# Kernel optimization log

Hardware: AMD Instinct MI355X
Metric: run time of the kernel (lower is better)

## Reference

```python
import math
import jax, jax.numpy as jnp
import numpy as np

N_HEAD = 16
HEAD_DIM = 128


def _rope(x, cos, sin):
    # x: (B,T,H,D); cos,sin: (T,1,D/2) broadcast over B,H
    d = x.shape[-1] // 2
    x1, x2 = x[..., :d], x[..., d:]
    return jnp.concatenate([x1 * cos + x2 * sin, -x1 * sin + x2 * cos], axis=-1)


def _rms_norm(x, eps=1e-6):
    return x * jax.lax.rsqrt(jnp.mean(x * x, axis=-1, keepdims=True) + eps)


def setup_inputs() -> dict:
    key = jax.random.key(0)
    ks = jax.random.split(key, 9)
    B, T, C = 2, 2048, 2048
    scale = 1.0 / math.sqrt(C)
    return {
        "x": jax.random.normal(ks[0], (B, T, C), jnp.float32),
        "ve": jax.random.normal(ks[1], (B, T, C), jnp.float32),
        "Wq": jax.random.normal(ks[2], (C, C), jnp.float32) * scale,
        "Wk": jax.random.normal(ks[3], (C, C), jnp.float32) * scale,
        "Wv": jax.random.normal(ks[4], (C, C), jnp.float32) * scale,
        "Wproj": jax.random.normal(ks[5], (C, C), jnp.float32) * scale,
        "Wgate": jax.random.normal(ks[6], (N_HEAD, 12), jnp.float32) * (1.0 / math.sqrt(12.0)),
        "cos": jax.random.uniform(ks[7], (T, 1, HEAD_DIM // 2), jnp.float32),
        "sin": jax.random.uniform(ks[8], (T, 1, HEAD_DIM // 2), jnp.float32),
        "window_left": 1024,
    }


def reference(x, ve, Wq, Wk, Wv, Wproj, Wgate, cos, sin, window_left):
    B, T, C = x.shape
    H, D = N_HEAD, HEAD_DIM

    # Linear projections (torch Linear: x @ W.T)
    q = (x @ Wq.T).reshape(B, T, H, D)
    k = (x @ Wk.T).reshape(B, T, H, D)
    v = (x @ Wv.T).reshape(B, T, H, D)

    # value-embedding gating (has_ve layer)
    gate = 3.0 * jax.nn.sigmoid(x[..., :12] @ Wgate.T)  # (B,T,H)
    v = v + gate[..., None] * ve.reshape(B, T, H, D)

    # rope + qk rms-norm * 1.2
    q = _rms_norm(_rope(q, cos, sin)) * 1.2
    k = _rms_norm(_rope(k, cos, sin)) * 1.2

    # windowed causal mask
    row = jnp.arange(T)[:, None]
    col = jnp.arange(T)[None, :]
    mask = row >= col
    if 0 < window_left < T:
        mask = mask & (row - col <= window_left)
    bias = jnp.where(mask, 0.0, -1e9).astype(x.dtype)  # (T,T)

    scale = 1.0 / math.sqrt(D)
    att = jnp.einsum("bqhd,bkhd->bhqk", q, k) * scale + bias[None, None]
    att = jax.nn.softmax(att, axis=-1)
    y = jnp.einsum("bhqk,bkhd->bqhd", att, v).reshape(B, T, H * D)
    return y @ Wproj.T
```

## Files before the change

### kernel.cpp

```cpp
#include <hip/hip_runtime.h>
#include <hip/hip_bf16.h>
#include <cstdint>

#define N_HEAD 16
#define HEAD_DIM 128

typedef __bf16 bf16;
typedef __bf16 bf16x8 __attribute__((ext_vector_type(8)));
typedef __bf16 bf16x4 __attribute__((ext_vector_type(4)));
typedef float f32x4 __attribute__((ext_vector_type(4)));

__device__ __forceinline__ void gload_lds16(const void* g, void* l) {
  auto gp = reinterpret_cast<const __attribute__((address_space(1))) char*>(
      reinterpret_cast<uintptr_t>(g));
  auto lp = reinterpret_cast<__attribute__((address_space(3))) char*>(
      reinterpret_cast<uintptr_t>(l));
  __builtin_amdgcn_global_load_lds(gp, lp, 16, 0, 0);
}

__global__ __launch_bounds__(256) void cvt_all(
    const float* __restrict__ x, const float* __restrict__ Wq,
    const float* __restrict__ Wk, const float* __restrict__ Wv,
    const float* __restrict__ Wp, bf16* __restrict__ xb,
    bf16* __restrict__ wqkv, bf16* __restrict__ wpb, int nx4, int nw4) {
  const int z = blockIdx.z;
  const float* in;
  bf16* out;
  int n4;
  if (z == 0)      { in = x;  out = xb;  n4 = nx4; }
  else if (z == 1) { in = Wq; out = wqkv;                     n4 = nw4; }
  else if (z == 2) { in = Wk; out = wqkv + (size_t)nw4 * 4;   n4 = nw4; }
  else if (z == 3) { in = Wv; out = wqkv + (size_t)nw4 * 8;   n4 = nw4; }
  else             { in = Wp; out = wpb;  n4 = nw4; }
  const int i = blockIdx.x * 256 + threadIdx.x;
  if (i >= n4) return;
  const float4 f = reinterpret_cast<const float4*>(in)[i];
  bf16x4 o;
  o.x = (bf16)f.x; o.y = (bf16)f.y; o.z = (bf16)f.z; o.w = (bf16)f.w;
  reinterpret_cast<bf16x4*>(out)[i] = o;
}

__global__ __launch_bounds__(512, 2) void gemm256(
    const bf16* __restrict__ A, const bf16* __restrict__ Bt,
    bf16* __restrict__ C, int M, int N, int K) {
  __shared__ __align__(16) char sA[2][32768];
  __shared__ __align__(16) char sB[2][32768];

  const int nwgy = M >> 8;
  const int nwg = gridDim.x;
  const int q8 = nwg >> 3;
  const int wgid = (blockIdx.x & 7) * q8 + (blockIdx.x >> 3);
  const int by = wgid % nwgy;
  const int bx = wgid / nwgy;

  const int tid = threadIdx.x;
  const int lane = tid & 63;
  const int wave = tid >> 6;
  const int wm = (wave >> 2) << 7;
  const int wn = (wave & 3) << 6;
  const int lr = lane & 15;
  const int lk16 = (lane >> 4) << 4;
  const int sx = (lr & 7) << 4;

  const bf16* Ab = A + (size_t)by * 256 * K;
  const bf16* Bb = Bt + (size_t)bx * 256 * K;

  int srow[2], scol[2];
#pragma unroll
  for (int pp = 0; pp < 2; ++pp) {
    const int o = pp * 8192 + tid * 16;
    srow[pp] = o >> 7;
    scol[pp] = (o & 127) ^ ((srow[pp] & 7) << 4);
  }

  auto stageA = [&](int buf, int half, int k0) {
#pragma unroll
    for (int pp = 0; pp < 2; ++pp)
      gload_lds16(Ab + (size_t)(half * 128 + srow[pp]) * K + k0 + (scol[pp] >> 1),
                  sA[buf] + half * 16384 + pp * 8192 + tid * 16);
  };
  auto stageB = [&](int buf, int half, int k0) {
#pragma unroll
    for (int pp = 0; pp < 2; ++pp)
      gload_lds16(Bb + (size_t)(half * 128 + srow[pp]) * K + k0 + (scol[pp] >> 1),
                  sB[buf] + half * 16384 + pp * 8192 + tid * 16);
  };

  f32x4 acc[8][4] = {};
  bf16x8 bF[4][2];

#define VMCNT4                                             \
  asm volatile("s_waitcnt vmcnt(4)" ::: "memory");         \
  __builtin_amdgcn_sched_barrier(0)
#define VMCNT0                                             \
  asm volatile("s_waitcnt vmcnt(0)" ::: "memory");         \
  __builtin_amdgcn_sched_barrier(0)

#define PHASE(BUF, P, STAGE, WAIT)                                             \
  {                                                                            \
    bf16x8 aF[2][2];                                                           \
    if (P == 0) {                                                              \
      _Pragma("unroll") for (int n = 0; n < 4; ++n)                            \
      _Pragma("unroll") for (int ks = 0; ks < 2; ++ks)                         \
        bF[n][ks] = *reinterpret_cast<const bf16x8*>(                          \
            sB[BUF] + (wn + n * 16 + lr) * 128 + ((ks * 64 + lk16) ^ sx));     \
    }                                                                          \
    _Pragma("unroll") for (int mi = 0; mi < 2; ++mi)                           \
    _Pragma("unroll") for (int ks = 0; ks < 2; ++ks)                           \
      aF[mi][ks] = *reinterpret_cast<const bf16x8*>(                           \
          sA[BUF] + (wm + (P * 2 + mi) * 16 + lr) * 128 +                      \
          ((ks * 64 + lk16) ^ sx));                                            \
    STAGE;                                                                     \
    WAIT;                                                                      \
    __builtin_amdgcn_s_barrier();                                              \
    __builtin_amdgcn_s_setprio(1);                                             \
    _Pragma("unroll") for (int ks = 0; ks < 2; ++ks)                           \
    _Pragma("unroll") for (int mi = 0; mi < 2; ++mi)                           \
    _Pragma("unroll") for (int n = 0; n < 4; ++n)                              \
      acc[P * 2 + mi][n] = __builtin_amdgcn_mfma_f32_16x16x32_bf16(            \
          aF[mi][ks], bF[n][ks], acc[P * 2 + mi][n], 0, 0, 0);                 \
    __builtin_amdgcn_s_setprio(0);                                             \
    __builtin_amdgcn_s_barrier();                                              \
  }

  const int nIt = K >> 7;

  stageB(0, 0, 0); stageB(0, 1, 0);
  stageA(0, 0, 0); stageA(0, 1, 0);
  stageB(1, 0, 64); stageB(1, 1, 64);
  VMCNT4;
  __builtin_amdgcn_s_barrier();

  int k0 = 0;
  for (int it = 0; it < nIt - 1; ++it, k0 += 128) {
    PHASE(0, 0, stageA(1, 0, k0 + 64), );
    PHASE(0, 1, stageA(1, 1, k0 + 64), );
    PHASE(0, 2, stageB(0, 0, k0 + 128), );
    PHASE(0, 3, stageB(0, 1, k0 + 128), VMCNT4);
    PHASE(1, 0, stageA(0, 0, k0 + 128), );
    PHASE(1, 1, stageA(0, 1, k0 + 128), );
    PHASE(1, 2, stageB(1, 0, k0 + 192), );
    PHASE(1, 3, stageB(1, 1, k0 + 192), VMCNT4);
  }
  PHASE(0, 0, stageA(1, 0, k0 + 64), );
  PHASE(0, 1, stageA(1, 1, k0 + 64), );
  PHASE(0, 2, , );
  PHASE(0, 3, , VMCNT0);
  PHASE(1, 0, , );
  PHASE(1, 1, , );
  PHASE(1, 2, , );
  PHASE(1, 3, , );
#undef PHASE
#undef VMCNT4
#undef VMCNT0

  const int orow = by * 256 + wm + (lane >> 4) * 4;
  const int ocol = bx * 256 + wn + lr;
#pragma unroll
  for (int m = 0; m < 8; ++m)
#pragma unroll
    for (int n = 0; n < 4; ++n)
#pragma unroll
      for (int r = 0; r < 4; ++r)
        C[(size_t)(orow + m * 16 + r) * N + (ocol + n * 16)] = (bf16)acc[m][n][r];
}

template <typename OutT>
__global__ __launch_bounds__(512, 2) void gemm128(
    const bf16* __restrict__ A, const bf16* __restrict__ Bt,
    OutT* __restrict__ C, int M, int Ncols, int K, int nOff) {
  __shared__ __align__(16) char sA[2][16384];
  __shared__ __align__(16) char sB[2][32768];

  const int nwgy = M >> 7;
  const int nwg = gridDim.x;
  const int q8 = nwg >> 3;
  const int wgid = (blockIdx.x & 7) * q8 + (blockIdx.x >> 3);
  const int by = wgid % nwgy;
  const int bx = wgid / nwgy;

  const int tid = threadIdx.x;
  const int lane = tid & 63;
  const int wave = tid >> 6;
  const int wn = wave << 5;
  const int lr = lane & 15;
  const int lk16 = (lane >> 4) << 4;
  const int sx = (lr & 7) << 4;

  const bf16* Ab = A + (size_t)by * 128 * K;
  const bf16* Bb = Bt + (size_t)(nOff + bx * 256) * K;

  int srow[2], scol[2];
#pragma unroll
  for (int pp = 0; pp < 2; ++pp) {
    const int o = pp * 8192 + tid * 16;
    srow[pp] = o >> 7;
    scol[pp] = (o & 127) ^ ((srow[pp] & 7) << 4);
  }

  auto stageB = [&](int buf, int half, int k0) {
#pragma unroll
    for (int pp = 0; pp < 2; ++pp)
      gload_lds16(Bb + (size_t)(half * 128 + srow[pp]) * K + k0 + (scol[pp] >> 1),
                  sB[buf] + half * 16384 + pp * 8192 + tid * 16);
  };
  auto stageA = [&](int buf, int half, int k0) {
    const int o = tid * 16;
    const int row = o >> 7;
    const int col = (o & 127) ^ ((row & 7) << 4);
    gload_lds16(Ab + (size_t)(half * 64 + row) * K + k0 + (col >> 1),
                sA[buf] + half * 8192 + o);
  };

  f32x4 acc[8][2] = {};
  bf16x8 bF[2][2];

#define WAITV(n)                                               \
  asm volatile("s_waitcnt vmcnt(" #n ")" ::: "memory");        \
  __builtin_amdgcn_sched_barrier(0)

#define PH128(BUF, P, STAGE, WAIT)                                             \
  {                                                                            \
    bf16x8 aF[2][2];                                                           \
    if (P == 0) {                                                              \
      _Pragma("unroll") for (int n = 0; n < 2; ++n)                            \
      _Pragma("unroll") for (int ks = 0; ks < 2; ++ks)                         \
        bF[n][ks] = *reinterpret_cast<const bf16x8*>(                          \
            sB[BUF] + (wn + n * 16 + lr) * 128 + ((ks * 64 + lk16) ^ sx));     \
    }                                                                          \
    _Pragma("unroll") for (int mi = 0; mi < 2; ++mi)                           \
    _Pragma("unroll") for (int ks = 0; ks < 2; ++ks)                           \
      aF[mi][ks] = *reinterpret_cast<const bf16x8*>(                           \
          sA[BUF] + ((P * 2 + mi) * 16 + lr) * 128 + ((ks * 64 + lk16) ^ sx)); \
    STAGE;                                                                     \
    WAIT;                                                                      \
    __builtin_amdgcn_s_barrier();                                              \
    __builtin_amdgcn_s_setprio(1);                                             \
    _Pragma("unroll") for (int ks = 0; ks < 2; ++ks)                           \
    _Pragma("unroll") for (int mi = 0; mi < 2; ++mi)                           \
    _Pragma("unroll") for (int n = 0; n < 2; ++n)                              \
      acc[P * 2 + mi][n] = __builtin_amdgcn_mfma_f32_16x16x32_bf16(            \
          aF[mi][ks], bF[n][ks], acc[P * 2 + mi][n], 0, 0, 0);                 \
    __builtin_amdgcn_s_setprio(0);                                             \
    __builtin_amdgcn_s_barrier();                                              \
  }

  const int nIt = K >> 7;

  stageB(0, 0, 0); stageB(0, 1, 0);
  stageA(0, 0, 0); stageA(0, 1, 0);
  stageB(1, 0, 64); stageB(1, 1, 64);
  stageA(1, 0, 64);
  WAITV(5);
  __builtin_amdgcn_s_barrier();

  int k0 = 0;
  for (int it = 0; it < nIt - 1; ++it, k0 += 128) {
    PH128(0, 0, stageA(1, 1, k0 + 64), );
    PH128(0, 1, stageB(0, 0, k0 + 128), WAITV(8));
    PH128(0, 2, (stageB(0, 1, k0 + 128), stageA(0, 0, k0 + 128)), );
    PH128(0, 3, , WAITV(6));
    PH128(1, 0, stageA(0, 1, k0 + 128), );
    PH128(1, 1, stageB(1, 0, k0 + 192), WAITV(8));
    PH128(1, 2, (stageB(1, 1, k0 + 192), stageA(1, 0, k0 + 192)), );
    PH128(1, 3, , WAITV(6));
  }
  PH128(0, 0, stageA(1, 1, k0 + 64), );
  PH128(0, 1, , WAITV(6));
  PH128(0, 2, , );
  PH128(0, 3, , WAITV(1));
  PH128(1, 0, , );
  PH128(1, 1, , WAITV(0));
  PH128(1, 2, , );
  PH128(1, 3, , );
#undef PH128
#undef WAITV

  const int orow = by * 128 + (lane >> 4) * 4;
  const int ocol = nOff + bx * 256 + wn + lr;
#pragma unroll
  for (int m = 0; m < 8; ++m)
#pragma unroll
    for (int n = 0; n < 2; ++n)
#pragma unroll
      for (int r = 0; r < 4; ++r)
        C[(size_t)(orow + m * 16 + r) * Ncols + (ocol + n * 16)] = (OutT)acc[m][n][r];
}

__global__ __launch_bounds__(256) void rope_rms(
    bf16* __restrict__ qkv, const float* __restrict__ cs,
    const float* __restrict__ sn, int T) {
  const int C = N_HEAD * HEAD_DIM;
  const int S = 3 * C;
  const int bt = blockIdx.x;
  const int t = bt % T;
  const int wave = threadIdx.x >> 6;
  const int lane = threadIdx.x & 63;
  const int h = blockIdx.y * 4 + wave;
  bf16* p = qkv + (size_t)bt * S + (blockIdx.z ? C : 0) + h * HEAD_DIM;
  const float oscale = blockIdx.z ? 1.2f : 0.15302091809294977f;
  const float c = cs[t * 64 + lane];
  const float s = sn[t * 64 + lane];
  const float x1 = (float)p[lane];
  const float x2 = (float)p[lane + 64];
  const float r1 = x1 * c + x2 * s;
  const float r2 = x2 * c - x1 * s;
  float ss = r1 * r1 + r2 * r2;
#pragma unroll
  for (int m = 1; m < 64; m <<= 1) ss += __shfl_xor(ss, m);
  const float sc = oscale * rsqrtf(ss * (1.0f / 128.0f) + 1e-6f);
  p[lane] = (bf16)(r1 * sc);
  p[lane + 64] = (bf16)(r2 * sc);
}

__global__ __launch_bounds__(256) void gate_transpose(
    const bf16* __restrict__ qkv, const float* __restrict__ x,
    const float* __restrict__ ve, const float* __restrict__ Wg,
    bf16* __restrict__ vT, int T) {
  const int C = N_HEAD * HEAD_DIM;
  const int S = 3 * C;
  const int t0 = blockIdx.x * 64;
  const int c0 = blockIdx.y * 64;
  const int b = blockIdx.z;
  const int h = c0 >> 7;

  __shared__ float gs[64];
  __shared__ __align__(16) bf16 tile[64][72];

  if (threadIdx.x < 64) {
    const float* xr = x + (size_t)(b * T + t0 + threadIdx.x) * C;
    float a = 0.f;
#pragma unroll
    for (int j = 0; j < 12; ++j) a += xr[j] * Wg[h * 12 + j];
    gs[threadIdx.x] = 3.f / (1.f + __expf(-a));
  }
  __syncthreads();

  {
    const int r = threadIdx.x >> 2;
    const int cc = (threadIdx.x & 3) * 16;
    const size_t vrow = (size_t)(b * T + t0 + r) * S + 2 * C + c0 + cc;
    const size_t erow = (size_t)(b * T + t0 + r) * C + c0 + cc;
    bf16x8 a0 = *reinterpret_cast<const bf16x8*>(qkv + vrow);
    bf16x8 a1 = *reinterpret_cast<const bf16x8*>(qkv + vrow + 8);
    const float g = gs[r];
    bf16x8 o0, o1;
#pragma unroll
    for (int i = 0; i < 8; ++i) o0[i] = (bf16)((float)a0[i] + g * ve[erow + i]);
#pragma unroll
    for (int i = 0; i < 8; ++i) o1[i] = (bf16)((float)a1[i] + g * ve[erow + 8 + i]);
    *reinterpret_cast<bf16x8*>(&tile[r][cc]) = o0;
    *reinterpret_cast<bf16x8*>(&tile[r][cc + 8]) = o1;
  }
  __syncthreads();
  {
    const int dr = threadIdx.x >> 2;
    const int tc = (threadIdx.x & 3) * 16;
    bf16x8 o0, o1;
#pragma unroll
    for (int i = 0; i < 8; ++i) o0[i] = tile[tc + i][dr];
#pragma unroll
    for (int i = 0; i < 8; ++i) o1[i] = tile[tc + 8 + i][dr];
    const size_t orow =
        ((size_t)((b * N_HEAD + h) * HEAD_DIM) + (c0 & 127) + dr) * T + t0 + tc;
    *reinterpret_cast<bf16x8*>(vT + orow) = o0;
    *reinterpret_cast<bf16x8*>(vT + orow + 8) = o1;
  }
}

__global__ __launch_bounds__(256, 2) void attn(
    const bf16* __restrict__ qkv, const bf16* __restrict__ vT,
    bf16* __restrict__ y, const int* __restrict__ wptr, int T, int B) {
  const int C = N_HEAD * HEAD_DIM;
  const int S = 3 * C;
  const int nq = T >> 7;
  const int ppx = (B * N_HEAD) >> 3;
  const int bid = blockIdx.x;
  const int xcd = bid & 7;
  const int sl = bid >> 3;
  const int pair = xcd * ppx + sl / nq;
  const int qi = sl % nq;
  const int b = pair / N_HEAD;
  const int h = pair % N_HEAD;
  const int qb = qi * 128;

  const int tid = threadIdx.x;
  const int wave = tid >> 6;
  const int lane = tid & 63;
  const int lm = lane & 15;
  const int quad = lane >> 4;

  const int w = wptr[0];
  const int W = (w > 0 && w < T) ? w : (1 << 30);

  __shared__ __align__(16) bf16 Ks[4][64][32];
  __shared__ __align__(16) bf16 Vs[2][128][32];
  __shared__ __align__(16) bf16 Pb[4][16][72];

  const bf16* kb = qkv + (size_t)b * T * S + C + (size_t)h * HEAD_DIM;
  const bf16* vb = vT + (size_t)((b * N_HEAD + h) * HEAD_DIM) * T;

  const int qt[2] = {qb + wave * 16, qb + 64 + wave * 16};
  bf16x8 qf[2][4];
#pragma unroll
  for (int t = 0; t < 2; ++t) {
    const bf16* qrow = qkv + (size_t)(b * T + qt[t] + lm) * S + h * HEAD_DIM;
#pragma unroll
    for (int c = 0; c < 4; ++c)
      qf[t][c] = *reinterpret_cast<const bf16x8*>(qrow + c * 32 + quad * 8);
  }

  float mrun[2] = {-1e30f, -1e30f}, lrun[2] = {0.f, 0.f};
  f32x4 oacc[2][8] = {};

  int kstart = qb - W;
  if (kstart < 0) kstart = 0;
  kstart &= ~63;
  const int kend = qb + 64;

  const int sr = tid >> 2;
  const int sc = (tid & 3) * 8;

  bf16x8 kpre[4], vpre[4];
  {
    const bf16* kr = kb + (size_t)(kstart + sr) * S + sc;
#pragma unroll
    for (int c = 0; c < 4; ++c)
      kpre[c] = *reinterpret_cast<const bf16x8*>(kr + c * 32);
#pragma unroll
    for (int c2 = 0; c2 < 2; ++c2)
#pragma unroll
      for (int i = 0; i < 2; ++i)
        vpre[c2 * 2 + i] = *reinterpret_cast<const bf16x8*>(
            vb + (size_t)(i * 64 + sr) * T + kstart + c2 * 32 + sc);
  }

  for (int kc = kstart; kc <= kend; kc += 64) {
    __syncthreads();
#pragma unroll
    for (int c = 0; c < 4; ++c)
      *reinterpret_cast<bf16x8*>(&Ks[c][sr][sc]) = kpre[c];
#pragma unroll
    for (int c2 = 0; c2 < 2; ++c2)
#pragma unroll
      for (int i = 0; i < 2; ++i)
        *reinterpret_cast<bf16x8*>(&Vs[c2][i * 64 + sr][sc]) = vpre[c2 * 2 + i];
    __syncthreads();

    if (kc + 64 <= kend) {
      const int kc2 = kc + 64;
      const bf16* kr = kb + (size_t)(kc2 + sr) * S + sc;
#pragma unroll
      for (int c = 0; c < 4; ++c)
        kpre[c] = *reinterpret_cast<const bf16x8*>(kr + c * 32);
#pragma unroll
      for (int c2 = 0; c2 < 2; ++c2)
#pragma unroll
        for (int i = 0; i < 2; ++i)
          vpre[c2 * 2 + i] = *reinterpret_cast<const bf16x8*>(
              vb + (size_t)(i * 64 + sr) * T + kc2 + c2 * 32 + sc);
    }

#pragma unroll
    for (int t = 0; t < 2; ++t) {
      const int q0 = qt[t];
      if (kc > q0 + 15 || kc + 63 < q0 - W) continue;
      const int qr = q0 + lm;

      f32x4 st[4] = {};
#pragma unroll
      for (int g = 0; g < 4; ++g)
#pragma unroll
        for (int c = 0; c < 4; ++c) {
          const bf16x8 kf =
              *reinterpret_cast<const bf16x8*>(&Ks[c][g * 16 + lm][quad * 8]);
          st[g] = __builtin_amdgcn_mfma_f32_16x16x32_bf16(kf, qf[t][c], st[g], 0, 0, 0);
        }
      float mx = -1e30f;
#pragma unroll
      for (int g = 0; g < 4; ++g)
#pragma unroll
        for (int r = 0; r < 4; ++r) {
          const int key = kc + g * 16 + quad * 4 + r;
          const bool valid = (key <= qr) && (qr - key <= W);
          st[g][r] = valid ? st[g][r] : -1e30f;
          mx = fmaxf(mx, st[g][r]);
        }
      mx = fmaxf(mx, __shfl_xor(mx, 16));
      mx = fmaxf(mx, __shfl_xor(mx, 32));
      const float mnew = fmaxf(mrun[t], mx);
      const float alpha = __builtin_amdgcn_exp2f(mrun[t] - mnew);
      mrun[t] = mnew;
      float rs = 0.f;
#pragma unroll
      for (int g = 0; g < 4; ++g) {
        bf16x4 pk;
#pragma unroll
        for (int r = 0; r < 4; ++r) {
          const float p = __builtin_amdgcn_exp2f(st[g][r] - mnew);
          rs += p;
          pk[r] = (bf16)p;
        }
        *reinterpret_cast<bf16x4*>(&Pb[wave][lm][g * 16 + quad * 4]) = pk;
      }
      rs += __shfl_xor(rs, 16);
      rs += __shfl_xor(rs, 32);
      lrun[t] = lrun[t] * alpha + rs;
#pragma unroll
      for (int dc = 0; dc < 8; ++dc)
#pragma unroll
        for (int r = 0; r < 4; ++r) oacc[t][dc][r] *= alpha;
#pragma unroll
      for (int c2 = 0; c2 < 2; ++c2) {
        const bf16x8 pf =
            *reinterpret_cast<const bf16x8*>(&Pb[wave][lm][c2 * 32 + quad * 8]);
#pragma unroll
        for (int dc = 0; dc < 8; ++dc) {
          const bf16x8 vf =
              *reinterpret_cast<const bf16x8*>(&Vs[c2][dc * 16 + lm][quad * 8]);
          oacc[t][dc] = __builtin_amdgcn_mfma_f32_16x16x32_bf16(vf, pf, oacc[t][dc], 0, 0, 0);
        }
      }
    }
  }

#pragma unroll
  for (int t = 0; t < 2; ++t) {
    const float inv = 1.f / lrun[t];
    bf16* yr = y + (size_t)(b * T + qt[t] + lm) * C + h * HEAD_DIM;
#pragma unroll
    for (int dc = 0; dc < 8; ++dc) {
      bf16x4 o;
#pragma unroll
      for (int r = 0; r < 4; ++r) o[r] = (bf16)(oacc[t][dc][r] * inv);
      *reinterpret_cast<bf16x4*>(yr + dc * 16 + quad * 4) = o;
    }
  }
}

extern "C" void kernel_launch(void* const* d_in, const int* in_sizes, int n_in,
                              void* d_out, int out_size, void* d_ws, size_t ws_size,
                              hipStream_t stream) {
  const float* x  = (const float*)d_in[0];
  const float* ve = (const float*)d_in[1];
  const float* Wq = (const float*)d_in[2];
  const float* Wk = (const float*)d_in[3];
  const float* Wv = (const float*)d_in[4];
  const float* Wp = (const float*)d_in[5];
  const float* Wg = (const float*)d_in[6];
  const float* cs = (const float*)d_in[7];
  const float* sn = (const float*)d_in[8];
  const int*   wl = (const int*)d_in[9];
  float* out = (float*)d_out;

  const int C = N_HEAD * HEAD_DIM;
  const int T = in_sizes[7] / (HEAD_DIM / 2);
  const int B = in_sizes[0] / (T * C);
  const int M = B * T;

  bf16* xb   = (bf16*)d_ws;
  bf16* wqkv = xb   + (size_t)M * C;
  bf16* wpb  = wqkv + (size_t)3 * C * C;
  bf16* qkv  = wpb  + (size_t)C * C;
  bf16* ybuf = qkv  + (size_t)3 * M * C;
  bf16* vTb  = xb;

  const int nx4 = M * C / 4, nw4 = C * C / 4;
  cvt_all<<<dim3((nx4 + 255) / 256, 1, 5), 256, 0, stream>>>(
      x, Wq, Wk, Wv, Wp, xb, wqkv, wpb, nx4, nw4);

  gemm256<<<dim3((M / 256) * 16), 512, 0, stream>>>(xb, wqkv, qkv, M, 3 * C, C);
  gemm128<bf16><<<dim3((M / 128) * 8), 512, 0, stream>>>(
      xb, wqkv, qkv, M, 3 * C, C, 2 * C);

  rope_rms<<<dim3(M, N_HEAD / 4, 2), 256, 0, stream>>>(qkv, cs, sn, T);
  gate_transpose<<<dim3(T / 64, C / 64, B), 256, 0, stream>>>(qkv, x, ve, Wg, vTb, T);
  attn<<<dim3(B * N_HEAD * (T / 128)), 256, 0, stream>>>(qkv, vTb, ybuf, wl, T, B);

  gemm128<float><<<dim3((M / 128) * (C / 256)), 512, 0, stream>>>(
      ybuf, wpb, out, M, C, C, 0);
}
```

Baseline: 395.8 us.

## Share K/V LDS fragments across both query tiles and swizzle LDS layout

```diff
diff --git a/kernel.cpp b/kernel.cpp
--- a/kernel.cpp
+++ b/kernel.cpp
@@ -389,13 +389,14 @@
   const int lane = tid & 63;
   const int lm = lane & 15;
   const int quad = lane >> 4;
+  const int lmw = (lm & 7) << 3;
 
   const int w = wptr[0];
   const int W = (w > 0 && w < T) ? w : (1 << 30);
 
-  __shared__ __align__(16) bf16 Ks[4][64][32];
-  __shared__ __align__(16) bf16 Vs[2][128][32];
-  __shared__ __align__(16) bf16 Pb[4][16][72];
+  __shared__ __align__(16) bf16 Ks[64][128];
+  __shared__ __align__(16) bf16 Vs[128][64];
+  __shared__ __align__(16) bf16 Pb[4][2][16][64];
 
   const bf16* kb = qkv + (size_t)b * T * S + C + (size_t)h * HEAD_DIM;
   const bf16* vb = vT + (size_t)((b * N_HEAD + h) * HEAD_DIM) * T;
@@ -419,110 +420,149 @@
   const int kend = qb + 64;
 
   const int sr = tid >> 2;
-  const int sc = (tid & 3) * 8;
+  const int s4 = (tid & 3) * 8;
+  const int swz = (sr & 7) << 3;
 
   bf16x8 kpre[4], vpre[4];
   {
-    const bf16* kr = kb + (size_t)(kstart + sr) * S + sc;
+    const bf16* kr = kb + (size_t)(kstart + sr) * S;
 #pragma unroll
     for (int c = 0; c < 4; ++c)
-      kpre[c] = *reinterpret_cast<const bf16x8*>(kr + c * 32);
+      kpre[c] = *reinterpret_cast<const bf16x8*>(kr + c * 32 + s4);
 #pragma unroll
     for (int c2 = 0; c2 < 2; ++c2)
 #pragma unroll
       for (int i = 0; i < 2; ++i)
         vpre[c2 * 2 + i] = *reinterpret_cast<const bf16x8*>(
-            vb + (size_t)(i * 64 + sr) * T + kstart + c2 * 32 + sc);
+            vb + (size_t)(i * 64 + sr) * T + kstart + c2 * 32 + s4);
+  }
+
+#define SOFTMAX_PB(t, st)                                                   \
+  {                                                                         \
+    const int qr = qt[t] + lm;                                              \
+    float mx = -1e30f;                                                      \
+    _Pragma("unroll") for (int g = 0; g < 4; ++g)                           \
+    _Pragma("unroll") for (int r = 0; r < 4; ++r) {                         \
+      const int key = kc + g * 16 + quad * 4 + r;                           \
+      const bool valid = (unsigned)(qr - key) <= (unsigned)W;               \
+      st[g][r] = valid ? st[g][r] : -1e30f;                                 \
+      mx = fmaxf(mx, st[g][r]);                                             \
+    }                                                                       \
+    mx = fmaxf(mx, __shfl_xor(mx, 16));                                     \
+    mx = fmaxf(mx, __shfl_xor(mx, 32));                                     \
+    float alpha = 1.f;                                                      \
+    if (!__all(mx <= mrun[t])) {                                            \
+      const float mnew = fmaxf(mrun[t], mx);                                \
+      alpha = __builtin_amdgcn_exp2f(mrun[t] - mnew);                       \
+      mrun[t] = mnew;                                                       \
+      _Pragma("unroll") for (int dc = 0; dc < 8; ++dc)                      \
+      _Pragma("unroll") for (int r = 0; r < 4; ++r) oacc[t][dc][r] *= alpha;\
+    }                                                                       \
+    float rs = 0.f;                                                         \
+    _Pragma("unroll") for (int g = 0; g < 4; ++g) {                         \
+      bf16x4 pk;                                                            \
+      _Pragma("unroll") for (int r = 0; r < 4; ++r) {                       \
+        const float p = __builtin_amdgcn_exp2f(st[g][r] - mrun[t]);         \
+        rs += p;                                                            \
+        pk[r] = (bf16)p;                                                    \
+      }                                                                     \
+      *reinterpret_cast<bf16x4*>(                                           \
+          &Pb[wave][t][lm][((g * 16 + (quad >> 1) * 8) ^ lmw) +             \
+                           (quad & 1) * 4]) = pk;                           \
+    }                                                                       \
+    rs += __shfl_xor(rs, 16);                                               \
+    rs += __shfl_xor(rs, 32);                                               \
+    lrun[t] = lrun[t] * alpha + rs;                                         \
+  }
+
+#define SINGLE_PASS(t)                                                      \
+  {                                                                         \
+    f32x4 st[4] = {};                                                       \
+    _Pragma("unroll") for (int g = 0; g < 4; ++g)                           \
+    _Pragma("unroll") for (int c = 0; c < 4; ++c) {                         \
+      const bf16x8 kf = *reinterpret_cast<const bf16x8*>(                   \
+          &Ks[g * 16 + lm][(c * 32 + quad * 8) ^ lmw]);                     \
+      st[g] = __builtin_amdgcn_mfma_f32_16x16x32_bf16(kf, qf[t][c], st[g],  \
+                                                      0, 0, 0);             \
+    }                                                                       \
+    SOFTMAX_PB(t, st);                                                      \
+    _Pragma("unroll") for (int c2 = 0; c2 < 2; ++c2) {                      \
+      const bf16x8 pf = *reinterpret_cast<const bf16x8*>(                   \
+          &Pb[wave][t][lm][(c2 * 32 + quad * 8) ^ lmw]);                    \
+      _Pragma("unroll") for (int dc = 0; dc < 8; ++dc) {                    \
+        const bf16x8 vf = *reinterpret_cast<const bf16x8*>(                 \
+            &Vs[dc * 16 + lm][(c2 * 32 + quad * 8) ^ lmw]);                 \
+        oacc[t][dc] = __builtin_amdgcn_mfma_f32_16x16x32_bf16(              \
+            vf, pf, oacc[t][dc], 0, 0, 0);                                  \
+      }                                                                     \
+    }                                                                       \
   }
 
   for (int kc = kstart; kc <= kend; kc += 64) {
     __syncthreads();
 #pragma unroll
     for (int c = 0; c < 4; ++c)
-      *reinterpret_cast<bf16x8*>(&Ks[c][sr][sc]) = kpre[c];
+      *reinterpret_cast<bf16x8*>(&Ks[sr][(c * 32 + s4) ^ swz]) = kpre[c];
 #pragma unroll
     for (int c2 = 0; c2 < 2; ++c2)
 #pragma unroll
       for (int i = 0; i < 2; ++i)
-        *reinterpret_cast<bf16x8*>(&Vs[c2][i * 64 + sr][sc]) = vpre[c2 * 2 + i];
+        *reinterpret_cast<bf16x8*>(&Vs[i * 64 + sr][(c2 * 32 + s4) ^ swz]) =
+            vpre[c2 * 2 + i];
     __syncthreads();
 
     if (kc + 64 <= kend) {
       const int kc2 = kc + 64;
-      const bf16* kr = kb + (size_t)(kc2 + sr) * S + sc;
+      const bf16* kr = kb + (size_t)(kc2 + sr) * S;
 #pragma unroll
       for (int c = 0; c < 4; ++c)
-        kpre[c] = *reinterpret_cast<const bf16x8*>(kr + c * 32);
+        kpre[c] = *reinterpret_cast<const bf16x8*>(kr + c * 32 + s4);
 #pragma unroll
       for (int c2 = 0; c2 < 2; ++c2)
 #pragma unroll
         for (int i = 0; i < 2; ++i)
           vpre[c2 * 2 + i] = *reinterpret_cast<const bf16x8*>(
-              vb + (size_t)(i * 64 + sr) * T + kc2 + c2 * 32 + sc);
+              vb + (size_t)(i * 64 + sr) * T + kc2 + c2 * 32 + s4);
     }
 
-#pragma unroll
-    for (int t = 0; t < 2; ++t) {
-      const int q0 = qt[t];
-      if (kc > q0 + 15 || kc + 63 < q0 - W) continue;
-      const int qr = q0 + lm;
-
-      f32x4 st[4] = {};
+    const bool a0 = !(kc > qt[0] + 15 || kc + 63 < qt[0] - W);
+    const bool a1 = !(kc > qt[1] + 15 || kc + 63 < qt[1] - W);
+
+    if (a0 & a1) {
+      f32x4 s0[4] = {}, s1[4] = {};
 #pragma unroll
       for (int g = 0; g < 4; ++g)
 #pragma unroll
         for (int c = 0; c < 4; ++c) {
-          const bf16x8 kf =
-              *reinterpret_cast<const bf16x8*>(&Ks[c][g * 16 + lm][quad * 8]);
-          st[g] = __builtin_amdgcn_mfma_f32_16x16x32_bf16(kf, qf[t][c], st[g], 0, 0, 0);
+          const bf16x8 kf = *reinterpret_cast<const bf16x8*>(
+              &Ks[g * 16 + lm][(c * 32 + quad * 8) ^ lmw]);
+          s0[g] = __builtin_amdgcn_mfma_f32_16x16x32_bf16(kf, qf[0][c], s0[g], 0, 0, 0);
+          s1[g] = __builtin_amdgcn_mfma_f32_16x16x32_bf16(kf, qf[1][c], s1[g], 0, 0, 0);
         }
-      float mx = -1e30f;
-#pragma unroll
-      for (int g = 0; g < 4; ++g)
-#pragma unroll
-        for (int r = 0; r < 4; ++r) {
-          const int key = kc + g * 16 + quad * 4 + r;
-          const bool valid = (key <= qr) && (qr - key <= W);
-          st[g][r] = valid ? st[g][r] : -1e30f;
-          mx = fmaxf(mx, st[g][r]);
-        }
-      mx = fmaxf(mx, __shfl_xor(mx, 16));
-      mx = fmaxf(mx, __shfl_xor(mx, 32));
-      const float mnew = fmaxf(mrun[t], mx);
-      const float alpha = __builtin_amdgcn_exp2f(mrun[t] - mnew);
-      mrun[t] = mnew;
-      float rs = 0.f;
-#pragma unroll
-      for (int g = 0; g < 4; ++g) {
-        bf16x4 pk;
-#pragma unroll
-        for (int r = 0; r < 4; ++r) {
-          const float p = __builtin_amdgcn_exp2f(st[g][r] - mnew);
-          rs += p;
-          pk[r] = (bf16)p;
-        }
-        *reinterpret_cast<bf16x4*>(&Pb[wave][lm][g * 16 + quad * 4]) = pk;
-      }
-      rs += __shfl_xor(rs, 16);
-      rs += __shfl_xor(rs, 32);
-      lrun[t] = lrun[t] * alpha + rs;
-#pragma unroll
-      for (int dc = 0; dc < 8; ++dc)
-#pragma unroll
-        for (int r = 0; r < 4; ++r) oacc[t][dc][r] *= alpha;
+      SOFTMAX_PB(0, s0);
+      SOFTMAX_PB(1, s1);
 #pragma unroll
       for (int c2 = 0; c2 < 2; ++c2) {
-        const bf16x8 pf =
-            *reinterpret_cast<const bf16x8*>(&Pb[wave][lm][c2 * 32 + quad * 8]);
+        const bf16x8 pf0 = *reinterpret_cast<const bf16x8*>(
+            &Pb[wave][0][lm][(c2 * 32 + quad * 8) ^ lmw]);
+        const bf16x8 pf1 = *reinterpret_cast<const bf16x8*>(
+            &Pb[wave][1][lm][(c2 * 32 + quad * 8) ^ lmw]);
 #pragma unroll
         for (int dc = 0; dc < 8; ++dc) {
-          const bf16x8 vf =
-              *reinterpret_cast<const bf16x8*>(&Vs[c2][dc * 16 + lm][quad * 8]);
-          oacc[t][dc] = __builtin_amdgcn_mfma_f32_16x16x32_bf16(vf, pf, oacc[t][dc], 0, 0, 0);
+          const bf16x8 vf = *reinterpret_cast<const bf16x8*>(
+              &Vs[dc * 16 + lm][(c2 * 32 + quad * 8) ^ lmw]);
+          oacc[0][dc] = __builtin_amdgcn_mfma_f32_16x16x32_bf16(vf, pf0, oacc[0][dc], 0, 0, 0);
+          oacc[1][dc] = __builtin_amdgcn_mfma_f32_16x16x32_bf16(vf, pf1, oacc[1][dc], 0, 0, 0);
         }
       }
+    } else if (a0) {
+      SINGLE_PASS(0);
+    } else if (a1) {
+      SINGLE_PASS(1);
     }
   }
+#undef SINGLE_PASS
+#undef SOFTMAX_PB
 
 #pragma unroll
   for (int t = 0; t < 2; ++t) {
```

Result: no change. 390.8 us (-1.3%).
